# Kernel optimization log

Hardware: AMD Instinct MI355X
Metric: run time of the kernel (lower is better)

The kernel has to match this reference:

```python
import jax, jax.numpy as jnp
import numpy as np

NEG_SLOPE = 0.2
LN_EPS = 1e-5


def _layer_norm(x, w, b):
    mu = jnp.mean(x, axis=-1, keepdims=True)
    var = jnp.mean((x - mu) ** 2, axis=-1, keepdims=True)
    return (x - mu) / jnp.sqrt(var + LN_EPS) * w + b


def setup_inputs() -> dict:
    N, E, R, H, D, HID, FF = 50000, 800000, 8, 4, 32, 128, 512
    key = jax.random.key(0)
    ks = jax.random.split(key, 12)
    s_w = float(np.sqrt(2.0 / (HID + HID)))  # xavier-ish scale
    return {
        "x": jax.random.normal(ks[0], (N, HID), jnp.float32),
        "weight": jax.random.normal(ks[1], (R, HID, HID), jnp.float32) * s_w,
        "root_weight": jax.random.normal(ks[2], (HID, HID), jnp.float32) * s_w,
        "edge_emb_table": jax.random.normal(ks[3], (R, HID), jnp.float32) * 0.01,
        "att_src": jax.random.normal(ks[4], (1, H, D), jnp.float32) * 0.1,
        "att_dst": jax.random.normal(ks[5], (1, H, D), jnp.float32) * 0.1,
        "att_edge": jax.random.normal(ks[6], (1, H, D), jnp.float32) * 0.1,
        "bias": jnp.zeros((HID,), jnp.float32),
        "norm1_w": jnp.ones((HID,), jnp.float32),
        "norm1_b": jnp.zeros((HID,), jnp.float32),
        "norm2_w": jnp.ones((HID,), jnp.float32),
        "norm2_b": jnp.zeros((HID,), jnp.float32),
        "ffn_w1": jax.random.normal(ks[7], (HID, FF), jnp.float32) * float(np.sqrt(2.0 / (HID + FF))),
        "ffn_b1": jnp.zeros((FF,), jnp.float32),
        "ffn_w2": jax.random.normal(ks[8], (FF, HID), jnp.float32) * float(np.sqrt(2.0 / (HID + FF))),
        "ffn_b2": jnp.zeros((HID,), jnp.float32),
        "edge_index": jax.random.randint(ks[9], (2, E), 0, N, jnp.int32),
        "edge_type": jax.random.randint(ks[10], (E,), 0, R, jnp.int32),
    }


def _rgat_conv(h, edge_index, edge_type, weight, root_weight, edge_emb_table,
               att_src, att_dst, att_edge, bias):
    N = h.shape[0]
    R = weight.shape[0]
    H, D = att_src.shape[1], att_src.shape[2]
    # relation-wise projection: [R, N, H, D]
    x_r = jnp.einsum('ni,rio->rno', h, weight).reshape(R, N, H, D)
    src, dst = edge_index[0], edge_index[1]
    x_src = x_r[edge_type, src]            # [E, H, D]
    x_dst = x_r[edge_type, dst]            # [E, H, D]
    edge_emb = edge_emb_table[edge_type].reshape(-1, H, D)
    alpha = (x_src * att_src).sum(-1) + (x_dst * att_dst).sum(-1) + (edge_emb * att_edge).sum(-1)  # [E, H]
    alpha = jax.nn.leaky_relu(alpha, NEG_SLOPE)
    # segment softmax over destination nodes
    amax = jax.ops.segment_max(alpha, dst, num_segments=N)  # [N, H]
    amax = jnp.where(jnp.isfinite(amax), amax, 0.0)
    ex = jnp.exp(alpha - amax[dst])
    den = jax.ops.segment_sum(ex, dst, num_segments=N)
    alpha = ex / (den[dst] + 1e-16)
    # dropout is identity in eval mode
    msg = x_src * alpha[..., None]         # [E, H, D]
    out = jax.ops.segment_sum(msg, dst, num_segments=N).reshape(N, H * D)
    return out + h @ root_weight + bias


def reference(x, weight, root_weight, edge_emb_table, att_src, att_dst, att_edge,
              bias, norm1_w, norm1_b, norm2_w, norm2_b,
              ffn_w1, ffn_b1, ffn_w2, ffn_b2, edge_index, edge_type):
    h = _layer_norm(x, norm1_w, norm1_b)
    h = _rgat_conv(h, edge_index, edge_type, weight, root_weight, edge_emb_table,
                   att_src, att_dst, att_edge, bias)
    h = jax.nn.elu(h)
    x = x + h
    h = _layer_norm(x, norm2_w, norm2_b)
    h = jax.nn.gelu(h @ ffn_w1 + ffn_b1, approximate=False) @ ffn_w2 + ffn_b2
    return x + h
```

## Files before the change

### kernel.cpp

```cpp
#include <hip/hip_runtime.h>
#include <hip/hip_bf16.h>
#include <math.h>

#define HID 128
#define NH  4
#define HD  32
#define FFD 512
#define RR  8
#define SCAN_B 1024
#define NB_SH 6

typedef __attribute__((ext_vector_type(8))) short bf16x8;
typedef __attribute__((ext_vector_type(4))) float f32x4;
typedef unsigned short u16;
typedef unsigned long long u64;

static __device__ __forceinline__ float bf2f(u16 u) {
    union { unsigned int i; float f; } v; v.i = ((unsigned int)u) << 16; return v.f;
}
static __device__ __forceinline__ u16 f2bf(float f) {
    union { float f; unsigned int i; } v; v.f = f;
    unsigned int x = v.i;
    return (u16)((x + 0x7fffu + ((x >> 16) & 1u)) >> 16);
}

__global__ void zeroout_kernel(float* out, int n) {
    int i = blockIdx.x * 256 + threadIdx.x;
    if (i < n) out[i] = 0.f;
}

__global__ void init_kernel(float* acc, int* deg2, int* bcnt, int NN, int NBK, int zacc) {
    int i = blockIdx.x * 256 + threadIdx.x;
    if (zacc && i < NN * HID) acc[i] = 0.f;
    if (i < NN * RR) deg2[i] = 0;
    if (i < NBK * 16) bcnt[i] = 0;
}

__global__ void stats_kernel(const float* in, float* mu, float* rs, int NN) {
    int row = blockIdx.x * 4 + (threadIdx.x >> 6);
    int lane = threadIdx.x & 63;
    if (row >= NN) return;
    const float* p = in + (size_t)row * HID;
    float v0 = p[lane], v1 = p[lane + 64];
    float s = v0 + v1;
    #pragma unroll
    for (int o = 32; o > 0; o >>= 1) s += __shfl_xor(s, o, 64);
    float m = s * (1.0f / HID);
    float d0 = v0 - m, d1 = v1 - m;
    float q = d0 * d0 + d1 * d1;
    #pragma unroll
    for (int o = 32; o > 0; o >>= 1) q += __shfl_xor(q, o, 64);
    if (lane == 0) { mu[row] = m; rs[row] = rsqrtf(q * (1.0f / HID) + 1e-5f); }
}

static __device__ __forceinline__
void hnorm_body(int idx, const float* in, const float* mu, const float* rs,
                const float* lw, const float* lb, u16* out, int NN) {
    if (idx >= NN * (HID / 8)) return;
    int row = idx >> 4;
    int k0 = (idx & 15) * 8;
    float m = mu[row], r = rs[row];
    const float* p = in + (size_t)row * HID + k0;
    float4 a0 = *(const float4*)p, a1 = *(const float4*)(p + 4);
    float4 w0 = *(const float4*)(lw + k0), w1 = *(const float4*)(lw + k0 + 4);
    float4 b0 = *(const float4*)(lb + k0), b1 = *(const float4*)(lb + k0 + 4);
    bf16x8 o;
    o[0] = (short)f2bf((a0.x - m) * r * w0.x + b0.x);
    o[1] = (short)f2bf((a0.y - m) * r * w0.y + b0.y);
    o[2] = (short)f2bf((a0.z - m) * r * w0.z + b0.z);
    o[3] = (short)f2bf((a0.w - m) * r * w0.w + b0.w);
    o[4] = (short)f2bf((a1.x - m) * r * w1.x + b1.x);
    o[5] = (short)f2bf((a1.y - m) * r * w1.y + b1.y);
    o[6] = (short)f2bf((a1.z - m) * r * w1.z + b1.z);
    o[7] = (short)f2bf((a1.w - m) * r * w1.w + b1.w);
    *(bf16x8*)(out + (size_t)row * HID + k0) = o;
}

__global__ void hnorm_kernel(const float* in, const float* mu, const float* rs,
                             const float* lw, const float* lb, u16* out, int NN) {
    hnorm_body(blockIdx.x * 256 + threadIdx.x, in, mu, rs, lw, lb, out, NN);
}

__global__ void transpose_kernel(const float* w, const float* rootw,
                                 const float* w1, const float* w2,
                                 u16* WT, u16* rootT, u16* W1T, u16* W2T, int R) {
    int i = blockIdx.x * 256 + threadIdx.x;
    int nW = R * HID * HID;
    if (i < nW) {
        int r = i / (HID * HID); int rem = i % (HID * HID);
        int n = rem / HID, k = rem % HID;
        WT[i] = f2bf(w[r * HID * HID + k * HID + n]);
    } else if (i < nW + HID * HID) {
        int j = i - nW; int n = j / HID, k = j % HID;
        rootT[j] = f2bf(rootw[k * HID + n]);
    } else if (i < nW + HID * HID + FFD * HID) {
        int j = i - nW - HID * HID; int n = j / HID, k = j % HID;
        W1T[j] = f2bf(w1[k * FFD + n]);
    } else if (i < nW + HID * HID + FFD * HID + HID * FFD) {
        int j = i - nW - HID * HID - FFD * HID; int n = j / FFD, k = j % FFD;
        W2T[j] = f2bf(w2[k * HID + n]);
    }
}

__global__ void vsd_kernel(const float* w, const float* att_src, const float* att_dst,
                           u16* Vsd, int R) {
    int idx = blockIdx.x * 256 + threadIdx.x;
    if (idx >= 64 * HID) return;
    int np = idx >> 7, k = idx & 127;
    int isDst = np >> 5, rh = np & 31, r = rh >> 2, h = rh & 3;
    const float* av = (isDst ? att_dst : att_src) + h * HD;
    const float* wp = w + (size_t)r * HID * HID + (size_t)k * HID + h * HD;
    float s = 0.f;
    #pragma unroll
    for (int d = 0; d < HD; d++) s += wp[d] * av[d];
    Vsd[idx] = f2bf(s);
}

__global__ void ae_kernel(const float* emb, const float* att_edge, float* ae, int R) {
    int i = threadIdx.x;
    if (i >= R * NH) return;
    int r = i >> 2, h = i & 3;
    float s = 0.f;
    #pragma unroll
    for (int d = 0; d < HD; d++)
        s += emb[r * HID + h * HD + d] * att_edge[h * HD + d];
    ae[i] = s;
}

template <int EPI, int TILED>
__global__ __launch_bounds__(256)
void gemmy_kernel(const u16* Araw, const u16* BT, u16* Cout, const float* bias,
                  int M, int N, int aOff, int cOff, int ytiles) {
    int w = threadIdx.x >> 6, lane = threadIdx.x & 63;
    int l15 = lane & 15, quad = lane >> 4;
    int m0 = blockIdx.x * 64 + w * 16;
    int rowA = m0 + l15; if (rowA > M - 1) rowA = M - 1;
    const u16* ap = Araw + (size_t)(aOff + rowA) * HID + quad * 8;
    bf16x8 a[4];
    #pragma unroll
    for (int kk = 0; kk < 4; kk++) a[kk] = *(const bf16x8*)(ap + kk * 32);

    __shared__ u16 tile[64][72];
    int rl2 = threadIdx.x >> 3, seg = threadIdx.x & 7;
    int ybase = blockIdx.y * ytiles;
    int nsub = N >> 6;
    for (int yi = 0; yi < ytiles; yi++) {
        int n0 = (ybase + yi) * 64;
        f32x4 accr[4] = {};
        #pragma unroll
        for (int kk = 0; kk < 4; kk++) {
            #pragma unroll
            for (int t = 0; t < 4; t++) {
                const u16* bp = BT + (size_t)(n0 + t * 16 + l15) * HID + quad * 8 + kk * 32;
                bf16x8 bfrag = *(const bf16x8*)bp;
                accr[t] = __builtin_amdgcn_mfma_f32_16x16x32_bf16(a[kk], bfrag, accr[t], 0, 0, 0);
            }
        }
        if (yi > 0) __syncthreads();
        #pragma unroll
        for (int t = 0; t < 4; t++) {
            int col = n0 + t * 16 + l15;
            #pragma unroll
            for (int j = 0; j < 4; j++) {
                float v = accr[t][j];
                if constexpr (EPI == 2) {
                    v += bias[col];
                    v = 0.5f * v * (1.0f + erff(v * 0.70710678118654752f));
                }
                tile[w * 16 + quad * 4 + j][t * 16 + l15] = f2bf(v);
            }
        }
        __syncthreads();
        if constexpr (TILED) {
            u16* tb = Cout + (((size_t)blockIdx.x * nsub + (ybase + yi)) << 12);
            #pragma unroll
            for (int h = 0; h < 2; h++) {
                int rl = h * 32 + rl2;
                int row = blockIdx.x * 64 + rl;
                if (row < M) {
                    *(bf16x8*)(tb + (rl << 6) + seg * 8) =
                        *(const bf16x8*)&tile[rl][seg * 8];
                }
            }
        } else {
            #pragma unroll
            for (int h = 0; h < 2; h++) {
                int rl = h * 32 + rl2;
                int row = blockIdx.x * 64 + rl;
                if (row < M) {
                    u16* dst = Cout + (size_t)(cOff + row) * N + n0 + seg * 8;
                    *(bf16x8*)dst = *(const bf16x8*)&tile[rl][seg * 8];
                }
            }
        }
    }
}

template <int AM, int EPI>
__global__ __launch_bounds__(256)
void gemm_kernel(const void* Araw, const float* mu, const float* rs,
                 const float* lw, const float* lb,
                 const u16* BT, void* Cout, const float* bias,
                 const float* acc, const float* xin, const float* invden,
                 int M, int N, int K, int aOff, int cOff) {
    int w = threadIdx.x >> 6, lane = threadIdx.x & 63;
    int l15 = lane & 15, quad = lane >> 4;
    int m0 = blockIdx.x * 64 + w * 16;
    int n0 = blockIdx.y * 64;
    int rowA = m0 + l15; if (rowA > M - 1) rowA = M - 1;
    int gA = aOff + rowA;
    float muv = 0.f, rsv = 0.f;
    if (AM != 2) { muv = mu[gA]; rsv = rs[gA]; }

    f32x4 accr[4] = {};
    for (int kc = 0; kc < K; kc += 32) {
        bf16x8 a;
        if (AM == 0) {
            const float* ap = (const float*)Araw + (size_t)gA * K + quad * 8 + kc;
            float4 xa0 = *(const float4*)(ap);
            float4 xa1 = *(const float4*)(ap + 4);
            float4 w0 = *(const float4*)(lw + kc + quad * 8);
            float4 w1v = *(const float4*)(lw + kc + quad * 8 + 4);
            float4 b0 = *(const float4*)(lb + kc + quad * 8);
            float4 b1v = *(const float4*)(lb + kc + quad * 8 + 4);
            a[0] = (short)f2bf((xa0.x - muv) * rsv * w0.x + b0.x);
            a[1] = (short)f2bf((xa0.y - muv) * rsv * w0.y + b0.y);
            a[2] = (short)f2bf((xa0.z - muv) * rsv * w0.z + b0.z);
            a[3] = (short)f2bf((xa0.w - muv) * rsv * w0.w + b0.w);
            a[4] = (short)f2bf((xa1.x - muv) * rsv * w1v.x + b1v.x);
            a[5] = (short)f2bf((xa1.y - muv) * rsv * w1v.y + b1v.y);
            a[6] = (short)f2bf((xa1.z - muv) * rsv * w1v.z + b1v.z);
            a[7] = (short)f2bf((xa1.w - muv) * rsv * w1v.w + b1v.w);
        } else {
            const u16* ap = (const u16*)Araw + (size_t)gA * K + quad * 8 + kc;
            a = *(const bf16x8*)ap;
        }
        #pragma unroll
        for (int t = 0; t < 4; t++) {
            const u16* bp = BT + (size_t)(n0 + t * 16 + l15) * K + quad * 8 + kc;
            bf16x8 bfrag = *(const bf16x8*)bp;
            accr[t] = __builtin_amdgcn_mfma_f32_16x16x32_bf16(a, bfrag, accr[t], 0, 0, 0);
        }
    }

    if constexpr (EPI == 0 || EPI == 2) {
        __shared__ u16 tile[64][72];
        #pragma unroll
        for (int t = 0; t < 4; t++) {
            int col = n0 + t * 16 + l15;
            #pragma unroll
            for (int j = 0; j < 4; j++) {
                float v = accr[t][j];
                if (EPI == 2) {
                    v += bias[col];
                    v = 0.5f * v * (1.0f + erff(v * 0.70710678118654752f));
                }
                tile[w * 16 + quad * 4 + j][t * 16 + l15] = f2bf(v);
            }
        }
        __syncthreads();
        int rl2 = threadIdx.x >> 3, seg = threadIdx.x & 7;
        #pragma unroll
        for (int h = 0; h < 2; h++) {
            int rl = h * 32 + rl2;
            int row = blockIdx.x * 64 + rl;
            if (row < M) {
                u16* dst = (u16*)Cout + (size_t)(cOff + row) * N + n0 + seg * 8;
                *(bf16x8*)dst = *(const bf16x8*)&tile[rl][seg * 8];
            }
        }
    } else {
        #pragma unroll
        for (int t = 0; t < 4; t++) {
            int col = n0 + t * 16 + l15;
            #pragma unroll
            for (int j = 0; j < 4; j++) {
                int row = m0 + quad * 4 + j;
                if (row < M) {
                    float v = accr[t][j];
                    int grow = cOff + row;
                    size_t off = (size_t)grow * N + col;
                    if (EPI == 1) {
                        float msg = acc[(size_t)grow * HID + col]
                                  * invden[(size_t)grow * NH + (col >> 5)];
                        float o = v + msg + bias[col];
                        o = o > 0.f ? o : expm1f(o);
                        ((float*)Cout)[off] = xin[off] + o;
                    } else if (EPI == 3) {
                        ((float*)Cout)[off] = v + bias[col] + xin[off];
                    } else if (EPI == 5) {
                        float* tab = (float*)Cout;
                        if (col < 32) tab[(size_t)grow * 32 + col] = v;
                        else tab[(size_t)(M + grow) * 32 + (col - 32)] = v;
                    }
                }
            }
        }
    }
}

__global__ void deg_kernel(const int* ei, const int* et, int* deg2, int E, int NN) {
    int e = blockIdx.x * 256 + threadIdx.x;
    if (e >= E) return;
    int s = ei[e], d = ei[E + e], r = et[e];
    if ((unsigned)d < (unsigned)NN && (unsigned)r < (unsigned)RR &&
        (unsigned)s < (unsigned)NN)
        atomicAdd(&deg2[d * RR + r], 1);
}

__global__ void scan1_kernel(const int* in, int* out, int* bsum, int n) {
    __shared__ int buf[SCAN_B];
    int i = blockIdx.x * SCAN_B + threadIdx.x;
    int v = (i < n) ? in[i] : 0;
    buf[threadIdx.x] = v;
    __syncthreads();
    for (int s = 1; s < SCAN_B; s <<= 1) {
        int t = (threadIdx.x >= s) ? buf[threadIdx.x - s] : 0;
        __syncthreads();
        buf[threadIdx.x] += t;
        __syncthreads();
    }
    if (i < n) out[i] = buf[threadIdx.x] - v;
    if (threadIdx.x == SCAN_B - 1) bsum[blockIdx.x] = buf[SCAN_B - 1];
}

__global__ void scan2_kernel(int* bsum, int nb) {
    __shared__ int buf[SCAN_B];
    int v = (threadIdx.x < nb) ? bsum[threadIdx.x] : 0;
    buf[threadIdx.x] = v;
    __syncthreads();
    for (int s = 1; s < SCAN_B; s <<= 1) {
        int t = (threadIdx.x >= s) ? buf[threadIdx.x - s] : 0;
        __syncthreads();
        buf[threadIdx.x] += t;
        __syncthreads();
    }
    if (threadIdx.x < nb) bsum[threadIdx.x] = buf[threadIdx.x] - v;
    if (threadIdx.x == SCAN_B - 1) bsum[nb] = buf[SCAN_B - 1];
}

__global__ void scan3_kernel(int* out, int* curpos, const int* bsum, int n, int nb) {
    int i = blockIdx.x * SCAN_B + threadIdx.x;
    if (i < n) {
        int o = out[i] + bsum[blockIdx.x];
        out[i] = o; curpos[i] = o;
    }
    if (i == 0) out[n] = bsum[nb];
}

static __device__ __forceinline__
void fillA_body(int e, const int* ei, const int* et, const int* offs2,
                int* bcnt, u64* tmp, int E, int NN) {
    if (e >= E) return;
    int s = ei[e], d = ei[E + e], r = et[e];
    if ((unsigned)d >= (unsigned)NN || (unsigned)r >= (unsigned)RR ||
        (unsigned)s >= (unsigned)NN) return;
    int b = d >> NB_SH;
    int base = offs2[(b << NB_SH) * RR];
    int pos = atomicAdd(&bcnt[b * 16], 1);
    tmp[base + pos] = ((u64)d << 32) | (unsigned)((r << 24) | s);
}

__global__ void fillA_kernel(const int* ei, const int* et, const int* offs2,
                             int* bcnt, u64* tmp, int E, int NN) {
    fillA_body(blockIdx.x * 256 + threadIdx.x, ei, et, offs2, bcnt, tmp, E, NN);
}

__global__ void fillB_kernel(const u64* tmp, const int* offs2,
                             int* curpos2, int* rs_arr, int NN) {
    int b = blockIdx.x;
    int n0 = b << NB_SH;
    int n1 = n0 + (1 << NB_SH); if (n1 > NN) n1 = NN;
    int base = offs2[n0 * RR];
    int end  = offs2[n1 * RR];
    for (int i = base + threadIdx.x; i < end; i += 256) {
        u64 t = tmp[i];
        int d = (int)(t >> 32);
        unsigned v = (unsigned)t;
        int r = v >> 24;
        int pos = atomicAdd(&curpos2[d * RR + r], 1);
        rs_arr[pos] = (int)v;
    }
}

static __device__ __forceinline__
void wgt_body(int n, const int* offs2, const int* rs_arr,
              const float* asad, const float* ae,
              float* wgtb, float* invden, int NN) {
    if (n >= NN) return;
    int lane = threadIdx.x & 63;
    int el = lane >> 2, h = lane & 3;
    int p0 = offs2[n * RR], p1 = offs2[n * RR + RR];
    const float* ad = asad + (size_t)NN * 32;
    float base[RR];
    #pragma unroll
    for (int r = 0; r < RR; r++)
        base[r] = ad[(size_t)n * 32 + r * 4 + h] + ae[r * 4 + h];
    float mx = -1e30f;
    for (int p = p0 + el; p < p1; p += 16) {
        unsigned v = (unsigned)rs_arr[p];
        int r = v >> 24, s = v & 0xFFFFFF;
        float a = asad[(size_t)s * 32 + r * 4 + h] + base[r];
        a = a > 0.f ? a : 0.2f * a;
        wgtb[(size_t)p * NH + h] = a;
        mx = fmaxf(mx, a);
    }
    #pragma unroll
    for (int o = 4; o < 64; o <<= 1) mx = fmaxf(mx, __shfl_xor(mx, o, 64));
    float den = 0.f;
    for (int p = p0 + el; p < p1; p += 16) {
        float ex = __expf(wgtb[(size_t)p * NH + h] - mx);
        wgtb[(size_t)p * NH + h] = ex;
        den += ex;
    }
    #pragma unroll
    for (int o = 4; o < 64; o <<= 1) den += __shfl_xor(den, o, 64);
    if (el == 0) invden[n * NH + h] = 1.0f / (den + 1e-16f);
}

__global__ void wgt_kernel(const int* offs2, const int* rs_arr,
                           const float* asad, const float* ae,
                           float* wgtb, float* invden, int NN, int E) {
    wgt_body(blockIdx.x * 4 + (threadIdx.x >> 6), offs2, rs_arr, asad, ae,
             wgtb, invden, NN);
}

__global__ __launch_bounds__(256)
void fused1_kernel(const float* x, const float* mu, const float* rs,
                   const float* lw, const float* lb, const u16* Vsd, float* asad,
                   u16* hb,
                   const int* ei, const int* et, const int* offs2,
                   int* bcnt, u64* tmp, int E, int NN, int gxN, int hB) {
    int bid = blockIdx.x;
    if (bid < gxN) {
        int w = threadIdx.x >> 6, lane = threadIdx.x & 63;
        int l15 = lane & 15, quad = lane >> 4;
        int m0 = bid * 64 + w * 16;
        int rowA = m0 + l15; if (rowA > NN - 1) rowA = NN - 1;
        float muv = mu[rowA], rsv = rs[rowA];
        f32x4 accr[4] = {};
        for (int kc = 0; kc < HID; kc += 32) {
            const float* ap = x + (size_t)rowA * HID + quad * 8 + kc;
            float4 xa0 = *(const float4*)(ap);
            float4 xa1 = *(const float4*)(ap + 4);
            float4 w0 = *(const float4*)(lw + kc + quad * 8);
            float4 w1v = *(const float4*)(lw + kc + quad * 8 + 4);
            float4 b0 = *(const float4*)(lb + kc + quad * 8);
            float4 b1v = *(const float4*)(lb + kc + quad * 8 + 4);
            bf16x8 a;
            a[0] = (short)f2bf((xa0.x - muv) * rsv * w0.x + b0.x);
            a[1] = (short)f2bf((xa0.y - muv) * rsv * w0.y + b0.y);
            a[2] = (short)f2bf((xa0.z - muv) * rsv * w0.z + b0.z);
            a[3] = (short)f2bf((xa0.w - muv) * rsv * w0.w + b0.w);
            a[4] = (short)f2bf((xa1.x - muv) * rsv * w1v.x + b1v.x);
            a[5] = (short)f2bf((xa1.y - muv) * rsv * w1v.y + b1v.y);
            a[6] = (short)f2bf((xa1.z - muv) * rsv * w1v.z + b1v.z);
            a[7] = (short)f2bf((xa1.w - muv) * rsv * w1v.w + b1v.w);
            #pragma unroll
            for (int t = 0; t < 4; t++) {
                const u16* bp = Vsd + (size_t)(t * 16 + l15) * HID + quad * 8 + kc;
                bf16x8 bfrag = *(const bf16x8*)bp;
                accr[t] = __builtin_amdgcn_mfma_f32_16x16x32_bf16(a, bfrag, accr[t], 0, 0, 0);
            }
        }
        #pragma unroll
        for (int t = 0; t < 4; t++) {
            int col = t * 16 + l15;
            #pragma unroll
            for (int j = 0; j < 4; j++) {
                int row = m0 + quad * 4 + j;
                if (row < NN) {
                    float v = accr[t][j];
                    if (col < 32) asad[(size_t)row * 32 + col] = v;
                    else asad[(size_t)(NN + row) * 32 + (col - 32)] = v;
                }
            }
        }
    } else if (bid < gxN + hB) {
        hnorm_body((bid - gxN) * 256 + threadIdx.x, x, mu, rs, lw, lb, hb, NN);
    } else {
        fillA_body((bid - gxN - hB) * 256 + threadIdx.x, ei, et, offs2,
                   bcnt, tmp, E, NN);
    }
}

__global__ __launch_bounds__(256)
void fused2_kernel(const u16* hb, const u16* WTw, u16* xp,
                   const int* offs2, const int* rs_arr, const float* asad,
                   const float* ae, float* wgtb, float* invden,
                   int NN, int gxN, int projB) {
    __shared__ u16 tile[64][72];
    int bid = blockIdx.x;
    if (bid < projB) {
        int xb = bid % gxN, yb = bid / gxN;
        int w = threadIdx.x >> 6, lane = threadIdx.x & 63;
        int l15 = lane & 15, quad = lane >> 4;
        int m0 = xb * 64 + w * 16;
        int rowA = m0 + l15; if (rowA > NN - 1) rowA = NN - 1;
        const u16* ap = hb + (size_t)rowA * HID + quad * 8;
        bf16x8 a[4];
        #pragma unroll
        for (int kk = 0; kk < 4; kk++) a[kk] = *(const bf16x8*)(ap + kk * 32);
        int rl2 = threadIdx.x >> 3, seg = threadIdx.x & 7;
        int ybase = yb * 8;
        for (int yi = 0; yi < 8; yi++) {
            int n0 = (ybase + yi) * 64;
            f32x4 accr[4] = {};
            #pragma unroll
            for (int kk = 0; kk < 4; kk++) {
                #pragma unroll
                for (int t = 0; t < 4; t++) {
                    const u16* bp = WTw + (size_t)(n0 + t * 16 + l15) * HID + quad * 8 + kk * 32;
                    bf16x8 bfrag = *(const bf16x8*)bp;
                    accr[t] = __builtin_amdgcn_mfma_f32_16x16x32_bf16(a[kk], bfrag, accr[t], 0, 0, 0);
                }
            }
            if (yi > 0) __syncthreads();
            #pragma unroll
            for (int t = 0; t < 4; t++) {
                #pragma unroll
                for (int j = 0; j < 4; j++) {
                    tile[w * 16 + quad * 4 + j][t * 16 + l15] = f2bf(accr[t][j]);
                }
            }
            __syncthreads();
            u16* tb = xp + (((size_t)xb * 16 + (ybase + yi)) << 12);
            #pragma unroll
            for (int h = 0; h < 2; h++) {
                int rl = h * 32 + rl2;
                int row = xb * 64 + rl;
                if (row < NN) {
                    *(bf16x8*)(tb + (rl << 6) + seg * 8) =
                        *(const bf16x8*)&tile[rl][seg * 8];
                }
            }
        }
    } else {
        wgt_body((bid - projB) * 4 + (threadIdx.x >> 6), offs2, rs_arr,
                 asad, ae, wgtb, invden, NN);
    }
}

__global__ __launch_bounds__(256)
void msg1_kernel(const int* offs2, const int* rs_arr, const float* wgt,
                 const u16* xp, float* acc, int NN) {
    int n = blockIdx.x * 4 + (threadIdx.x >> 6);
    if (n >= NN) return;
    int lane = threadIdx.x & 63;
    int half = lane >> 5;
    int co = (lane & 31) << 1;
    int h = lane >> 4;
    int p0 = offs2[n * RR], p1 = offs2[n * RR + RR];
    float a0 = 0.f, a1 = 0.f;
    int p = p0;
    for (; p + 4 <= p1; p += 4) {
        unsigned v0 = (unsigned)rs_arr[p + 0];
        unsigned v1 = (unsigned)rs_arr[p + 1];
        unsigned v2 = (unsigned)rs_arr[p + 2];
        unsigned v3 = (unsigned)rs_arr[p + 3];
        unsigned s0 = v0 & 0xFFFFFFu, s1 = v1 & 0xFFFFFFu;
        unsigned s2 = v2 & 0xFFFFFFu, s3 = v3 & 0xFFFFFFu;
        unsigned z0 = *(const unsigned*)(xp
            + (((size_t)(s0 >> 6) * 16 + ((v0 >> 24) << 1) + half) << 12)
            + ((s0 & 63) << 6) + co);
        unsigned z1 = *(const unsigned*)(xp
            + (((size_t)(s1 >> 6) * 16 + ((v1 >> 24) << 1) + half) << 12)
            + ((s1 & 63) << 6) + co);
        unsigned z2 = *(const unsigned*)(xp
            + (((size_t)(s2 >> 6) * 16 + ((v2 >> 24) << 1) + half) << 12)
            + ((s2 & 63) << 6) + co);
        unsigned z3 = *(const unsigned*)(xp
            + (((size_t)(s3 >> 6) * 16 + ((v3 >> 24) << 1) + half) << 12)
            + ((s3 & 63) << 6) + co);
        float w0 = wgt[(size_t)(p + 0) * NH + h];
        float w1 = wgt[(size_t)(p + 1) * NH + h];
        float w2 = wgt[(size_t)(p + 2) * NH + h];
        float w3 = wgt[(size_t)(p + 3) * NH + h];
        a0 += w0 * bf2f((u16)z0) + w1 * bf2f((u16)z1)
            + w2 * bf2f((u16)z2) + w3 * bf2f((u16)z3);
        a1 += w0 * bf2f((u16)(z0 >> 16)) + w1 * bf2f((u16)(z1 >> 16))
            + w2 * bf2f((u16)(z2 >> 16)) + w3 * bf2f((u16)(z3 >> 16));
    }
    for (; p < p1; p++) {
        unsigned v = (unsigned)rs_arr[p];
        unsigned s = v & 0xFFFFFFu;
        unsigned z = *(const unsigned*)(xp
            + (((size_t)(s >> 6) * 16 + ((v >> 24) << 1) + half) << 12)
            + ((s & 63) << 6) + co);
        float wv = wgt[(size_t)p * NH + h];
        a0 += wv * bf2f((u16)z);
        a1 += wv * bf2f((u16)(z >> 16));
    }
    float2 o; o.x = a0; o.y = a1;
    *(float2*)(acc + (size_t)n * HID + (lane << 1)) = o;
}

__global__ void msg2_kernel(const int* offs2, const int* rs_arr, const float* wgt,
                            const u16* xp, float* acc, int rc, int nrel, int ldx,
                            int NN, int E) {
    int n = blockIdx.x;
    int c = threadIdx.x, h = c >> 5;
    int p0 = offs2[n * RR + rc], p1 = offs2[n * RR + rc + nrel];
    if (p0 >= p1) return;
    float av = acc[(size_t)n * HID + c];
    for (int p = p0; p < p1; p++) {
        unsigned v = (unsigned)rs_arr[p];
        int r = (v >> 24) - rc;
        int s = v & 0xFFFFFF;
        av += wgt[(size_t)p * NH + h] * bf2f(xp[(size_t)s * ldx + r * HID + c]);
    }
    acc[(size_t)n * HID + c] = av;
}

extern "C" void kernel_launch(void* const* d_in, const int* in_sizes, int n_in,
                              void* d_out, int out_size, void* d_ws, size_t ws_size,
                              hipStream_t stream) {
    const float* x        = (const float*)d_in[0];
    const float* w        = (const float*)d_in[1];
    const float* rootw    = (const float*)d_in[2];
    const float* emb      = (const float*)d_in[3];
    const float* att_src  = (const float*)d_in[4];
    const float* att_dst  = (const float*)d_in[5];
    const float* att_edge = (const float*)d_in[6];
    const float* bias     = (const float*)d_in[7];
    const float* n1w      = (const float*)d_in[8];
    const float* n1b      = (const float*)d_in[9];
    const float* n2w      = (const float*)d_in[10];
    const float* n2b      = (const float*)d_in[11];
    const float* w1       = (const float*)d_in[12];
    const float* b1       = (const float*)d_in[13];
    const float* w2       = (const float*)d_in[14];
    const float* b2       = (const float*)d_in[15];
    const int* ei = (const int*)d_in[16];
    const int* et = (const int*)d_in[17];

    int NN = in_sizes[0] / HID;
    int R  = in_sizes[1] / (HID * HID);
    int E  = in_sizes[17];
    int NR = NN * RR;
    int NBK = (NN + (1 << NB_SH) - 1) >> NB_SH;
    int gxN = (NN + 63) / 64;
    int Mpad = gxN * 64;

    char* p = (char*)d_ws;
    auto alloc = [&](size_t bytes) -> char* {
        char* q = p; p += (bytes + 255) & ~(size_t)255; return q;
    };
    int* offs2   = (int*)alloc((size_t)(NR + 1) * 4);
    int* rs_arr  = (int*)alloc((size_t)E * 4);
    u16* WTw   = (u16*)alloc((size_t)R * HID * HID * 2);
    u16* rootT = (u16*)alloc((size_t)HID * HID * 2);
    u16* W1T   = (u16*)alloc((size_t)FFD * HID * 2);
    u16* W2T   = (u16*)alloc((size_t)HID * FFD * 2);
    u16* Vsd   = (u16*)alloc((size_t)64 * HID * 2);
    float* ae  = (float*)alloc((size_t)R * NH * 4);
    float* mu1 = (float*)alloc((size_t)NN * 4);
    float* rs1 = (float*)alloc((size_t)NN * 4);
    float* mu2 = (float*)alloc((size_t)NN * 4);
    float* rs2 = (float*)alloc((size_t)NN * 4);
    float* asad   = (float*)alloc((size_t)NN * 64 * 4);
    float* invden = (float*)alloc((size_t)NN * NH * 4);
    float* wgt    = (float*)alloc((size_t)E * NH * 4);
    float* acc    = (float*)alloc((size_t)NN * HID * 4);

    int nbScan = (NR + SCAN_B - 1) / SCAN_B;
    int* deg2    = (int*)wgt;
    int* curpos2 = deg2 + NR;
    int* bsum    = curpos2 + NR;
    int* bcnt    = bsum + nbScan + 1;
    u64* tmp     = (u64*)(((size_t)(bcnt + NBK * 16) + 7) & ~(size_t)7);

    size_t usedFixed = (size_t)(p - (char*)d_ws);
    size_t xpTiled = (size_t)Mpad * HID * RR * 2;
    size_t hbufSz  = (size_t)NN * HID * 2;
    int mode; int nrel = RR;
    u16 *xp, *hbuf;
    if (ws_size >= usedFixed + hbufSz + xpTiled + 512) {
        mode = 2;
        hbuf = (u16*)alloc(hbufSz);
        xp = (u16*)alloc(xpTiled);
    } else if (ws_size >= usedFixed + xpTiled + 256) {
        mode = 1;
        hbuf = (u16*)asad;
        xp = (u16*)alloc(xpTiled);
    } else {
        mode = 0;
        nrel = 1;
        for (int t = 4; t > 1; t >>= 1) {
            if (ws_size >= usedFixed + (size_t)NN * HID * t * 2 + 256) { nrel = t; break; }
        }
        hbuf = (u16*)asad;
        xp = (u16*)alloc((size_t)NN * HID * nrel * 2);
    }
    u16* u_ch = xp;
    float* x2 = (float*)d_out;

    size_t used = (size_t)(p - (char*)d_ws);
    if (used > ws_size) {
        zeroout_kernel<<<(out_size + 255) / 256, 256, 0, stream>>>((float*)d_out, out_size);
        return;
    }

    int initN = (mode != 0) ? (NR > NBK * 16 ? NR : NBK * 16) : NN * HID;
    init_kernel<<<(initN + 255) / 256, 256, 0, stream>>>(acc, deg2, bcnt, NN, NBK,
                                                         mode == 0 ? 1 : 0);
    stats_kernel<<<(NN + 3) / 4, 256, 0, stream>>>(x, mu1, rs1, NN);
    int nT = R * HID * HID + HID * HID + FFD * HID + HID * FFD;
    transpose_kernel<<<(nT + 255) / 256, 256, 0, stream>>>(w, rootw, w1, w2,
                                                           WTw, rootT, W1T, W2T, R);
    vsd_kernel<<<(64 * HID + 255) / 256, 256, 0, stream>>>(w, att_src, att_dst, Vsd, R);
    ae_kernel<<<1, 64, 0, stream>>>(emb, att_edge, ae, R);
    deg_kernel<<<(E + 255) / 256, 256, 0, stream>>>(ei, et, deg2, E, NN);
    scan1_kernel<<<nbScan, SCAN_B, 0, stream>>>(deg2, offs2, bsum, NR);
    scan2_kernel<<<1, SCAN_B, 0, stream>>>(bsum, nbScan);
    scan3_kernel<<<nbScan, SCAN_B, 0, stream>>>(offs2, curpos2, bsum, NR, nbScan);

    int hB = (NN * (HID / 8) + 255) / 256;
    int fB = (E + 255) / 256;

    if (mode == 2) {
        fused1_kernel<<<gxN + hB + fB, 256, 0, stream>>>(
            x, mu1, rs1, n1w, n1b, Vsd, asad, hbuf,
            ei, et, offs2, bcnt, tmp, E, NN, gxN, hB);
        fillB_kernel<<<NBK, 256, 0, stream>>>(tmp, offs2, curpos2, rs_arr, NN);
        int projB = gxN * 2;
        int wB = (NN + 3) / 4;
        fused2_kernel<<<projB + wB, 256, 0, stream>>>(
            hbuf, WTw, xp, offs2, rs_arr, asad, ae, wgt, invden, NN, gxN, projB);
        msg1_kernel<<<(NN + 3) / 4, 256, 0, stream>>>(offs2, rs_arr, wgt, xp, acc, NN);
    } else {
        fillA_kernel<<<fB, 256, 0, stream>>>(ei, et, offs2, bcnt, tmp, E, NN);
        fillB_kernel<<<NBK, 256, 0, stream>>>(tmp, offs2, curpos2, rs_arr, NN);
        gemm_kernel<0, 5><<<dim3(gxN, 1), 256, 0, stream>>>(
            x, mu1, rs1, n1w, n1b, Vsd, asad,
            nullptr, nullptr, nullptr, nullptr, NN, 64, HID, 0, 0);
        wgt_kernel<<<(NN + 3) / 4, 256, 0, stream>>>(
            offs2, rs_arr, asad, ae, wgt, invden, NN, E);
        hnorm_kernel<<<hB, 256, 0, stream>>>(x, mu1, rs1, n1w, n1b, hbuf, NN);
        if (mode == 1) {
            gemmy_kernel<0, 1><<<dim3(gxN, 2), 256, 0, stream>>>(
                hbuf, WTw, xp, nullptr, NN, HID * RR, 0, 0, 8);
            msg1_kernel<<<(NN + 3) / 4, 256, 0, stream>>>(offs2, rs_arr, wgt, xp, acc, NN);
        } else {
            for (int rc = 0; rc < RR; rc += nrel) {
                gemm_kernel<2, 0><<<dim3(gxN, (HID * nrel) / 64), 256, 0, stream>>>(
                    hbuf, nullptr, nullptr, nullptr, nullptr, WTw + (size_t)rc * HID * HID,
                    xp, nullptr, nullptr, nullptr, nullptr, NN, HID * nrel, HID, 0, 0);
                msg2_kernel<<<NN, HID, 0, stream>>>(offs2, rs_arr, wgt, xp, acc,
                                                    rc, nrel, HID * nrel, NN, E);
            }
        }
    }

    gemm_kernel<2, 1><<<dim3(gxN, HID / 64), 256, 0, stream>>>(
        hbuf, nullptr, nullptr, nullptr, nullptr, rootT, x2, bias, acc, x, invden,
        NN, HID, HID, 0, 0);

    stats_kernel<<<(NN + 3) / 4, 256, 0, stream>>>(x2, mu2, rs2, NN);
    hnorm_kernel<<<hB, 256, 0, stream>>>(x2, mu2, rs2, n2w, n2b, hbuf, NN);
    int nchunk = (mode != 0) ? 1 : (nrel >= 4 ? 1 : (nrel == 2 ? 2 : 4));
    int NCH = (NN + nchunk - 1) / nchunk;
    for (int j = 0; j < nchunk; j++) {
        int r0 = j * NCH;
        int Mc = NN - r0; if (Mc > NCH) Mc = NCH;
        if (Mc <= 0) continue;
        int gxc = (Mc + 63) / 64;
        gemmy_kernel<2, 0><<<dim3(gxc, 2), 256, 0, stream>>>(
            hbuf, W1T, u_ch, b1, Mc, FFD, r0, 0, 4);
        gemm_kernel<2, 3><<<dim3(gxc, HID / 64), 256, 0, stream>>>(
            u_ch, nullptr, nullptr, nullptr, nullptr, W2T, (float*)d_out, b2,
            nullptr, x2, nullptr, Mc, HID, FFD, 0, r0);
    }
}
```

Before: 588.1 us.

## Fuse root GEMM with message aggregation and merge epilogue with second layernorm

In the large-workspace path, the root-weight projection now runs as extra blocks inside the same launch as message aggregation, writing a bf16 result into a reused buffer. A new epilogue kernel then combines root projection, normalized messages, bias, ELU and the residual, and computes the second layernorm in one row pass. This replaces four separate launches (root GEMM, aggregation, stats, hnorm) and avoids rereading x2. In exchange, the root projection is rounded to bf16 before the add, and the GEMM blocks compete with the gather blocks for the GPU.

```diff
diff --git a/kernel.cpp b/kernel.cpp
--- a/kernel.cpp
+++ b/kernel.cpp
@@ -539,6 +539,140 @@
         wgt_body((bid - projB) * 4 + (threadIdx.x >> 6), offs2, rs_arr,
                  asad, ae, wgtb, invden, NN);
     }
+}
+
+__global__ __launch_bounds__(256)
+void fused3_kernel(const u16* hb, const u16* rootT, u16* rootp,
+                   const int* offs2, const int* rs_arr, const float* wgtb,
+                   const u16* xp, float* acc, int NN, int gxN) {
+    __shared__ u16 tile[64][72];
+    int bid = blockIdx.x;
+    if (bid < 2 * gxN) {
+        int xb = bid >> 1, yb = bid & 1;
+        int w = threadIdx.x >> 6, lane = threadIdx.x & 63;
+        int l15 = lane & 15, quad = lane >> 4;
+        int m0 = xb * 64 + w * 16;
+        int rowA = m0 + l15; if (rowA > NN - 1) rowA = NN - 1;
+        const u16* ap = hb + (size_t)rowA * HID + quad * 8;
+        bf16x8 a[4];
+        #pragma unroll
+        for (int kk = 0; kk < 4; kk++) a[kk] = *(const bf16x8*)(ap + kk * 32);
+        int n0 = yb * 64;
+        f32x4 accr[4] = {};
+        #pragma unroll
+        for (int kk = 0; kk < 4; kk++) {
+            #pragma unroll
+            for (int t = 0; t < 4; t++) {
+                const u16* bp = rootT + (size_t)(n0 + t * 16 + l15) * HID + quad * 8 + kk * 32;
+                bf16x8 bfrag = *(const bf16x8*)bp;
+                accr[t] = __builtin_amdgcn_mfma_f32_16x16x32_bf16(a[kk], bfrag, accr[t], 0, 0, 0);
+            }
+        }
+        #pragma unroll
+        for (int t = 0; t < 4; t++) {
+            #pragma unroll
+            for (int j = 0; j < 4; j++) {
+                tile[w * 16 + quad * 4 + j][t * 16 + l15] = f2bf(accr[t][j]);
+            }
+        }
+        __syncthreads();
+        int rl2 = threadIdx.x >> 3, seg = threadIdx.x & 7;
+        #pragma unroll
+        for (int h = 0; h < 2; h++) {
+            int rl = h * 32 + rl2;
+            int row = xb * 64 + rl;
+            if (row < NN) {
+                u16* dst = rootp + (size_t)row * HID + n0 + seg * 8;
+                *(bf16x8*)dst = *(const bf16x8*)&tile[rl][seg * 8];
+            }
+        }
+    } else {
+        int n = (bid - 2 * gxN) * 4 + (threadIdx.x >> 6);
+        if (n >= NN) return;
+        int lane = threadIdx.x & 63;
+        int half = lane >> 5;
+        int co = (lane & 31) << 1;
+        int h = lane >> 4;
+        int p0 = offs2[n * RR], p1 = offs2[n * RR + RR];
+        float a0 = 0.f, a1 = 0.f;
+        int p = p0;
+        for (; p + 4 <= p1; p += 4) {
+            unsigned v0 = (unsigned)rs_arr[p + 0];
+            unsigned v1 = (unsigned)rs_arr[p + 1];
+            unsigned v2 = (unsigned)rs_arr[p + 2];
+            unsigned v3 = (unsigned)rs_arr[p + 3];
+            unsigned s0 = v0 & 0xFFFFFFu, s1 = v1 & 0xFFFFFFu;
+            unsigned s2 = v2 & 0xFFFFFFu, s3 = v3 & 0xFFFFFFu;
+            unsigned z0 = *(const unsigned*)(xp
+                + (((size_t)(s0 >> 6) * 16 + ((v0 >> 24) << 1) + half) << 12)
+                + ((s0 & 63) << 6) + co);
+            unsigned z1 = *(const unsigned*)(xp
+                + (((size_t)(s1 >> 6) * 16 + ((v1 >> 24) << 1) + half) << 12)
+                + ((s1 & 63) << 6) + co);
+            unsigned z2 = *(const unsigned*)(xp
+                + (((size_t)(s2 >> 6) * 16 + ((v2 >> 24) << 1) + half) << 12)
+                + ((s2 & 63) << 6) + co);
+            unsigned z3 = *(const unsigned*)(xp
+                + (((size_t)(s3 >> 6) * 16 + ((v3 >> 24) << 1) + half) << 12)
+                + ((s3 & 63) << 6) + co);
+            float w0 = wgtb[(size_t)(p + 0) * NH + h];
+            float w1 = wgtb[(size_t)(p + 1) * NH + h];
+            float w2 = wgtb[(size_t)(p + 2) * NH + h];
+            float w3 = wgtb[(size_t)(p + 3) * NH + h];
+            a0 += w0 * bf2f((u16)z0) + w1 * bf2f((u16)z1)
+                + w2 * bf2f((u16)z2) + w3 * bf2f((u16)z3);
+            a1 += w0 * bf2f((u16)(z0 >> 16)) + w1 * bf2f((u16)(z1 >> 16))
+                + w2 * bf2f((u16)(z2 >> 16)) + w3 * bf2f((u16)(z3 >> 16));
+        }
+        for (; p < p1; p++) {
+            unsigned v = (unsigned)rs_arr[p];
+            unsigned s = v & 0xFFFFFFu;
+            unsigned z = *(const unsigned*)(xp
+                + (((size_t)(s >> 6) * 16 + ((v >> 24) << 1) + half) << 12)
+                + ((s & 63) << 6) + co);
+            float wv = wgtb[(size_t)p * NH + h];
+            a0 += wv * bf2f((u16)z);
+            a1 += wv * bf2f((u16)(z >> 16));
+        }
+        float2 o; o.x = a0; o.y = a1;
+        *(float2*)(acc + (size_t)n * HID + (lane << 1)) = o;
+    }
+}
+
+__global__ __launch_bounds__(256)
+void epi2_kernel(const u16* rootp, const float* acc, const float* invden,
+                 const float* bias, const float* x, float* x2,
+                 const float* n2w, const float* n2b, u16* hb, int NN) {
+    int row = blockIdx.x * 4 + (threadIdx.x >> 6);
+    if (row >= NN) return;
+    int lane = threadIdx.x & 63;
+    int c2 = lane << 1;
+    unsigned rp = *(const unsigned*)(rootp + (size_t)row * HID + c2);
+    float2 av = *(const float2*)(acc + (size_t)row * HID + c2);
+    float inv = invden[row * NH + (lane >> 4)];
+    float2 bv = *(const float2*)(bias + c2);
+    float2 xv = *(const float2*)(x + (size_t)row * HID + c2);
+    float o0 = bf2f((u16)rp) + av.x * inv + bv.x;
+    float o1 = bf2f((u16)(rp >> 16)) + av.y * inv + bv.y;
+    o0 = o0 > 0.f ? o0 : expm1f(o0);
+    o1 = o1 > 0.f ? o1 : expm1f(o1);
+    float v0 = xv.x + o0, v1 = xv.y + o1;
+    float2 ov; ov.x = v0; ov.y = v1;
+    *(float2*)(x2 + (size_t)row * HID + c2) = ov;
+    float s = v0 + v1;
+    #pragma unroll
+    for (int o = 32; o > 0; o >>= 1) s += __shfl_xor(s, o, 64);
+    float m = s * (1.0f / HID);
+    float d0 = v0 - m, d1 = v1 - m;
+    float q = d0 * d0 + d1 * d1;
+    #pragma unroll
+    for (int o = 32; o > 0; o >>= 1) q += __shfl_xor(q, o, 64);
+    float rsv = rsqrtf(q * (1.0f / HID) + 1e-5f);
+    float2 wv = *(const float2*)(n2w + c2);
+    float2 b2v = *(const float2*)(n2b + c2);
+    unsigned pk = (unsigned)f2bf(d0 * rsv * wv.x + b2v.x)
+                | ((unsigned)f2bf(d1 * rsv * wv.y + b2v.y) << 16);
+    *(unsigned*)(hb + (size_t)row * HID + c2) = pk;
 }
 
 __global__ __launch_bounds__(256)
@@ -693,6 +827,7 @@
         xp = (u16*)alloc((size_t)NN * HID * nrel * 2);
     }
     u16* u_ch = xp;
+    u16* rootp = (u16*)asad;
     float* x2 = (float*)d_out;
 
     size_t used = (size_t)(p - (char*)d_ws);
@@ -717,6 +852,7 @@
 
     int hB = (NN * (HID / 8) + 255) / 256;
     int fB = (E + 255) / 256;
+    int wB = (NN + 3) / 4;
 
     if (mode == 2) {
         fused1_kernel<<<gxN + hB + fB, 256, 0, stream>>>(
@@ -724,23 +860,25 @@
             ei, et, offs2, bcnt, tmp, E, NN, gxN, hB);
         fillB_kernel<<<NBK, 256, 0, stream>>>(tmp, offs2, curpos2, rs_arr, NN);
         int projB = gxN * 2;
-        int wB = (NN + 3) / 4;
         fused2_kernel<<<projB + wB, 256, 0, stream>>>(
             hbuf, WTw, xp, offs2, rs_arr, asad, ae, wgt, invden, NN, gxN, projB);
-        msg1_kernel<<<(NN + 3) / 4, 256, 0, stream>>>(offs2, rs_arr, wgt, xp, acc, NN);
+        fused3_kernel<<<2 * gxN + wB, 256, 0, stream>>>(
+            hbuf, rootT, rootp, offs2, rs_arr, wgt, xp, acc, NN, gxN);
+        epi2_kernel<<<wB, 256, 0, stream>>>(
+            rootp, acc, invden, bias, x, x2, n2w, n2b, hbuf, NN);
     } else {
         fillA_kernel<<<fB, 256, 0, stream>>>(ei, et, offs2, bcnt, tmp, E, NN);
         fillB_kernel<<<NBK, 256, 0, stream>>>(tmp, offs2, curpos2, rs_arr, NN);
         gemm_kernel<0, 5><<<dim3(gxN, 1), 256, 0, stream>>>(
             x, mu1, rs1, n1w, n1b, Vsd, asad,
             nullptr, nullptr, nullptr, nullptr, NN, 64, HID, 0, 0);
-        wgt_kernel<<<(NN + 3) / 4, 256, 0, stream>>>(
+        wgt_kernel<<<wB, 256, 0, stream>>>(
             offs2, rs_arr, asad, ae, wgt, invden, NN, E);
         hnorm_kernel<<<hB, 256, 0, stream>>>(x, mu1, rs1, n1w, n1b, hbuf, NN);
         if (mode == 1) {
             gemmy_kernel<0, 1><<<dim3(gxN, 2), 256, 0, stream>>>(
                 hbuf, WTw, xp, nullptr, NN, HID * RR, 0, 0, 8);
-            msg1_kernel<<<(NN + 3) / 4, 256, 0, stream>>>(offs2, rs_arr, wgt, xp, acc, NN);
+            msg1_kernel<<<wB, 256, 0, stream>>>(offs2, rs_arr, wgt, xp, acc, NN);
         } else {
             for (int rc = 0; rc < RR; rc += nrel) {
                 gemm_kernel<2, 0><<<dim3(gxN, (HID * nrel) / 64), 256, 0, stream>>>(
@@ -750,14 +888,13 @@
                                                     rc, nrel, HID * nrel, NN, E);
             }
         }
-    }
-
-    gemm_kernel<2, 1><<<dim3(gxN, HID / 64), 256, 0, stream>>>(
-        hbuf, nullptr, nullptr, nullptr, nullptr, rootT, x2, bias, acc, x, invden,
-        NN, HID, HID, 0, 0);
-
-    stats_kernel<<<(NN + 3) / 4, 256, 0, stream>>>(x2, mu2, rs2, NN);
-    hnorm_kernel<<<hB, 256, 0, stream>>>(x2, mu2, rs2, n2w, n2b, hbuf, NN);
+        gemm_kernel<2, 1><<<dim3(gxN, HID / 64), 256, 0, stream>>>(
+            hbuf, nullptr, nullptr, nullptr, nullptr, rootT, x2, bias, acc, x, invden,
+            NN, HID, HID, 0, 0);
+        stats_kernel<<<wB, 256, 0, stream>>>(x2, mu2, rs2, NN);
+        hnorm_kernel<<<hB, 256, 0, stream>>>(x2, mu2, rs2, n2w, n2b, hbuf, NN);
+    }
+
     int nchunk = (mode != 0) ? 1 : (nrel >= 4 ? 1 : (nrel == 2 ? 2 : 4));
     int NCH = (NN + nchunk - 1) / nchunk;
     for (int j = 0; j < nchunk; j++) {
```

New measurement: 575.2 us. 2.2% less time.
